# Performance work log

Hardware: AMD Instinct MI355X
Metric: run time of the kernel (lower is better)

## Reference

```python
import jax, jax.numpy as jnp
import numpy as np

B, T, C, H, L = 4, 1024, 1024, 16, 8
Dh = C // H
FF = 4 * C


def _build_mask():
    # init_mask with token_decoder='tokenlearner', prompt=False, block_size=T-1
    block_size = T - 1
    i = np.arange(T)[:, None]
    j = np.arange(T)[None, :]
    tril = j <= i
    # rows i < block_size additionally see cols j of the same 10-unit with j%10 in [0,8]
    unit = 10
    extra = (i < block_size) & (i // unit == j // unit) & (j % unit <= unit - 2)
    return jnp.asarray((tril | extra).astype(np.float32))


def setup_inputs() -> dict:
    key = jax.random.key(0)
    ks = jax.random.split(key, 16)
    s = 0.02
    d = {
        "x": jax.random.normal(ks[0], (B, T, C), jnp.float32),
        "ln1_w": jnp.ones((L, C), jnp.float32),
        "ln1_b": jnp.zeros((L, C), jnp.float32),
        "ln2_w": jnp.ones((L, C), jnp.float32),
        "ln2_b": jnp.zeros((L, C), jnp.float32),
        "wq": s * jax.random.normal(ks[1], (L, C, C), jnp.float32),
        "bq": jnp.zeros((L, C), jnp.float32),
        "wk": s * jax.random.normal(ks[2], (L, C, C), jnp.float32),
        "bk": jnp.zeros((L, C), jnp.float32),
        "wv": s * jax.random.normal(ks[3], (L, C, C), jnp.float32),
        "bv": jnp.zeros((L, C), jnp.float32),
        "wo": s * jax.random.normal(ks[4], (L, C, C), jnp.float32),
        "bo": jnp.zeros((L, C), jnp.float32),
        "w1": s * jax.random.normal(ks[5], (L, C, FF), jnp.float32),
        "b1": jnp.zeros((L, FF), jnp.float32),
        "w2": s * jax.random.normal(ks[6], (L, FF, C), jnp.float32),
        "b2": jnp.zeros((L, C), jnp.float32),
        "mask": _build_mask(),
    }
    return d


def _layer_norm(x, w, b):
    mu = jnp.mean(x, axis=-1, keepdims=True)
    var = jnp.mean(jnp.square(x - mu), axis=-1, keepdims=True)
    return (x - mu) * jax.lax.rsqrt(var + 1e-5) * w + b


def _gpt_stack(x, params, mask):
    neg = jnp.finfo(x.dtype).min
    keep = mask != 0.0  # [T, T]

    def block(xc, p):
        (ln1w, ln1b, ln2w, ln2b, wq, bq, wk, bk, wv, bv,
         wo, bo, w1, b1, w2, b2) = p
        h = _layer_norm(xc, ln1w, ln1b)
        q = (h @ wq + bq).reshape(B, T, H, Dh).transpose(0, 2, 1, 3)
        k = (h @ wk + bk).reshape(B, T, H, Dh).transpose(0, 2, 1, 3)
        v = (h @ wv + bv).reshape(B, T, H, Dh).transpose(0, 2, 1, 3)
        att = jnp.einsum('bhqd,bhkd->bhqk', q, k) * (1.0 / np.sqrt(Dh))
        att = jnp.where(keep[None, None], att, neg)
        att = jax.nn.softmax(att, axis=-1)
        y = jnp.einsum('bhqk,bhkd->bhqd', att, v)
        y = y.transpose(0, 2, 1, 3).reshape(B, T, C)
        xc = xc + y @ wo + bo
        h2 = _layer_norm(xc, ln2w, ln2b)
        m = jax.nn.gelu(h2 @ w1 + b1, approximate=False) @ w2 + b2
        return xc + m

    def step(carry, p):
        return block(carry, p), None

    out, _ = jax.lax.scan(step, x, params)
    return out


def reference(x, ln1_w, ln1_b, ln2_w, ln2_b, wq, bq, wk, bk, wv, bv,
              wo, bo, w1, b1, w2, b2, mask):
    params = (ln1_w, ln1_b, ln2_w, ln2_b, wq, bq, wk, bk, wv, bv,
              wo, bo, w1, b1, w2, b2)
    return _gpt_stack(x, params, mask)
```

## Files before the change

### kernel.cpp

```cpp
#include <hip/hip_runtime.h>

#define TT 1024
#define CC 1024
#define HH 16
#define DHH 64
#define BB 4
#define LL 8
#define FFF 4096
#define MM (BB*TT)

typedef float f32x4 __attribute__((ext_vector_type(4)));
typedef short s16x8 __attribute__((ext_vector_type(8)));
typedef unsigned short u16x8 __attribute__((ext_vector_type(8)));
typedef unsigned short u16x4 __attribute__((ext_vector_type(4)));

__device__ __forceinline__ unsigned short f2bf(float x) {
  unsigned int u = __float_as_uint(x);
  unsigned int r = u + 0x7FFFu + ((u >> 16) & 1u);
  return (unsigned short)(r >> 16);
}
__device__ __forceinline__ float bf2f(unsigned short h) {
  return __uint_as_float(((unsigned int)h) << 16);
}
__device__ __forceinline__ float gelu_f(float x) {
  return 0.5f * x * (1.0f + erff(x * 0.70710678118654752f));
}

struct SplitArgs {
  const float* src[6];
  unsigned short* dh[6];
  unsigned short* dl[6];
};

__global__ __launch_bounds__(256) void splitT_k(SplitArgs a) {
  __shared__ float Ls[64][65];
  int idx = blockIdx.x;
  int r, t;
  if (idx < 1024)      { r = idx >> 8; t = idx & 255; }
  else if (idx < 2048) { r = 4; t = idx - 1024; }
  else                 { r = 5; t = idx - 2048; }
  int K = (r == 5) ? FFF : CC;
  int N = (r == 4) ? FFF : CC;
  int Nt = N >> 6;
  int k0 = (t / Nt) * 64, n0 = (t % Nt) * 64;

  const float* s = a.src[r];
  int tid = threadIdx.x;
  int rrow = tid >> 4, rcol = tid & 15;
#pragma unroll
  for (int i = 0; i < 4; ++i) {
    int rl = rrow + 16 * i;
    float4 v = *(const float4*)(s + (size_t)(k0 + rl) * N + n0 + rcol * 4);
    Ls[rl][rcol * 4 + 0] = v.x; Ls[rl][rcol * 4 + 1] = v.y;
    Ls[rl][rcol * 4 + 2] = v.z; Ls[rl][rcol * 4 + 3] = v.w;
  }
  __syncthreads();

  int nl = tid >> 2, ks = (tid & 3) * 16;
  u16x8 h0, h1, l0, l1;
#pragma unroll
  for (int j = 0; j < 8; ++j) {
    float f = Ls[ks + j][nl];
    h0[j] = f2bf(f); l0[j] = f2bf(f - bf2f(h0[j]));
  }
#pragma unroll
  for (int j = 0; j < 8; ++j) {
    float f = Ls[ks + 8 + j][nl];
    h1[j] = f2bf(f); l1[j] = f2bf(f - bf2f(h1[j]));
  }
  size_t o = (size_t)(n0 + nl) * K + k0 + ks;
  *(u16x8*)(a.dh[r] + o) = h0; *(u16x8*)(a.dh[r] + o + 8) = h1;
  *(u16x8*)(a.dl[r] + o) = l0; *(u16x8*)(a.dl[r] + o + 8) = l1;
}

template <int OUT>
__global__ __launch_bounds__(256) void ln_k(const float* __restrict__ x,
                                            const float* __restrict__ w,
                                            const float* __restrict__ b,
                                            float* __restrict__ of,
                                            unsigned short* __restrict__ oh,
                                            unsigned short* __restrict__ ol) {
  int row = blockIdx.x;
  int tid = threadIdx.x;
  const float* xr = x + (size_t)row * CC;
  float4 v = ((const float4*)xr)[tid];
  float s = v.x + v.y + v.z + v.w;
#pragma unroll
  for (int m = 1; m < 64; m <<= 1) s += __shfl_xor(s, m, 64);
  __shared__ float r1[4];
  __shared__ float r2[4];
  if ((tid & 63) == 0) r1[tid >> 6] = s;
  __syncthreads();
  float mu = (r1[0] + r1[1] + r1[2] + r1[3]) * (1.0f / CC);
  float d0 = v.x - mu, d1 = v.y - mu, d2 = v.z - mu, d3 = v.w - mu;
  float sq = d0 * d0 + d1 * d1 + d2 * d2 + d3 * d3;
#pragma unroll
  for (int m = 1; m < 64; m <<= 1) sq += __shfl_xor(sq, m, 64);
  if ((tid & 63) == 0) r2[tid >> 6] = sq;
  __syncthreads();
  float var = (r2[0] + r2[1] + r2[2] + r2[3]) * (1.0f / CC);
  float rs = rsqrtf(var + 1e-5f);
  float4 wv = ((const float4*)w)[tid];
  float4 bv = ((const float4*)b)[tid];
  float o0 = d0 * rs * wv.x + bv.x;
  float o1 = d1 * rs * wv.y + bv.y;
  float o2 = d2 * rs * wv.z + bv.z;
  float o3 = d3 * rs * wv.w + bv.w;
  if (OUT == 0) {
    float4 ov; ov.x = o0; ov.y = o1; ov.z = o2; ov.w = o3;
    ((float4*)(of + (size_t)row * CC))[tid] = ov;
  } else {
    u16x4 h, lo;
    h[0] = f2bf(o0); lo[0] = f2bf(o0 - bf2f(h[0]));
    h[1] = f2bf(o1); lo[1] = f2bf(o1 - bf2f(h[1]));
    h[2] = f2bf(o2); lo[2] = f2bf(o2 - bf2f(h[2]));
    h[3] = f2bf(o3); lo[3] = f2bf(o3 - bf2f(h[3]));
    *(u16x4*)(oh + (size_t)row * CC + tid * 4) = h;
    *(u16x4*)(ol + (size_t)row * CC + tid * 4) = lo;
  }
}

#define LDA 40

template <int EPI>
__device__ __forceinline__ void sgemm_body(
    const unsigned short* __restrict__ Ah, const unsigned short* __restrict__ Al,
    const unsigned short* __restrict__ Bh, const unsigned short* __restrict__ Bl,
    const float* __restrict__ bias, const float* __restrict__ res,
    float* __restrict__ Cf, unsigned short* __restrict__ Ch,
    unsigned short* __restrict__ Cl,
    int M, int N, int K, int m0, int n0,
    unsigned short* sAh, unsigned short* sAl,
    unsigned short* sBh, unsigned short* sBl) {
  int tid = threadIdx.x;
  int lane = tid & 63;
  int w = tid >> 6;
  int wr = w >> 1, wc = w & 1;
  int l15 = lane & 15, l4 = lane >> 4;

  int sr = tid >> 1, skh = (tid & 1) * 16;
  const unsigned short* ApH = Ah + (size_t)(m0 + sr) * K + skh;
  const unsigned short* ApL = Al + (size_t)(m0 + sr) * K + skh;
  const unsigned short* BpH = Bh + (size_t)(n0 + sr) * K + skh;
  const unsigned short* BpL = Bl + (size_t)(n0 + sr) * K + skh;

  u16x8 rah0 = *(const u16x8*)ApH, rah1 = *(const u16x8*)(ApH + 8);
  u16x8 ral0 = *(const u16x8*)ApL, ral1 = *(const u16x8*)(ApL + 8);
  u16x8 rbh0 = *(const u16x8*)BpH, rbh1 = *(const u16x8*)(BpH + 8);
  u16x8 rbl0 = *(const u16x8*)BpL, rbl1 = *(const u16x8*)(BpL + 8);

  f32x4 acc[4][4];
#pragma unroll
  for (int i = 0; i < 4; ++i)
#pragma unroll
    for (int j = 0; j < 4; ++j) acc[i][j] = {0.f, 0.f, 0.f, 0.f};

  int soff = sr * LDA + skh;
  int nsteps = K >> 5;
  for (int s = 0; s < nsteps; ++s) {
    *(u16x8*)&sAh[soff] = rah0; *(u16x8*)&sAh[soff + 8] = rah1;
    *(u16x8*)&sAl[soff] = ral0; *(u16x8*)&sAl[soff + 8] = ral1;
    *(u16x8*)&sBh[soff] = rbh0; *(u16x8*)&sBh[soff + 8] = rbh1;
    *(u16x8*)&sBl[soff] = rbl0; *(u16x8*)&sBl[soff + 8] = rbl1;
    __syncthreads();

    if (s + 1 < nsteps) {
      int ko = (s + 1) * 32;
      rah0 = *(const u16x8*)(ApH + ko); rah1 = *(const u16x8*)(ApH + ko + 8);
      ral0 = *(const u16x8*)(ApL + ko); ral1 = *(const u16x8*)(ApL + ko + 8);
      rbh0 = *(const u16x8*)(BpH + ko); rbh1 = *(const u16x8*)(BpH + ko + 8);
      rbl0 = *(const u16x8*)(BpL + ko); rbl1 = *(const u16x8*)(BpL + ko + 8);
    }

    s16x8 afh[4], afl[4];
    int ab = (wr * 64 + l15) * LDA + 8 * l4;
#pragma unroll
    for (int mr = 0; mr < 4; ++mr) {
      afh[mr] = *(const s16x8*)&sAh[ab + mr * 16 * LDA];
      afl[mr] = *(const s16x8*)&sAl[ab + mr * 16 * LDA];
    }
    int bb = (wc * 64 + l15) * LDA + 8 * l4;
#pragma unroll
    for (int nr = 0; nr < 4; ++nr) {
      s16x8 bfh = *(const s16x8*)&sBh[bb + nr * 16 * LDA];
      s16x8 bfl = *(const s16x8*)&sBl[bb + nr * 16 * LDA];
#pragma unroll
      for (int mr = 0; mr < 4; ++mr) {
        acc[mr][nr] = __builtin_amdgcn_mfma_f32_16x16x32_bf16(afh[mr], bfh, acc[mr][nr], 0, 0, 0);
        acc[mr][nr] = __builtin_amdgcn_mfma_f32_16x16x32_bf16(afl[mr], bfh, acc[mr][nr], 0, 0, 0);
        acc[mr][nr] = __builtin_amdgcn_mfma_f32_16x16x32_bf16(afh[mr], bfl, acc[mr][nr], 0, 0, 0);
      }
    }
    __syncthreads();
  }

  int row0 = m0 + wr * 64 + l4 * 4;
  int col0 = n0 + wc * 64 + l15;
#pragma unroll
  for (int nr = 0; nr < 4; ++nr) {
    int col = col0 + nr * 16;
    float bv = bias[col];
#pragma unroll
    for (int mr = 0; mr < 4; ++mr) {
#pragma unroll
      for (int r = 0; r < 4; ++r) {
        int row = row0 + mr * 16 + r;
        size_t idx = (size_t)row * N + col;
        float v = acc[mr][nr][r] + bv;
        if (EPI == 0) Cf[idx] = v;
        if (EPI == 1) Cf[idx] = v + res[idx];
        if (EPI == 2) {
          float g = gelu_f(v);
          unsigned short hbits = f2bf(g);
          Ch[idx] = hbits;
          Cl[idx] = f2bf(g - bf2f(hbits));
        }
      }
    }
  }
}

template <int EPI>
__global__ __launch_bounds__(256) void sgemm_k(
    const unsigned short* Ah, const unsigned short* Al,
    const unsigned short* Bh, const unsigned short* Bl,
    const float* bias, const float* res,
    float* Cf, unsigned short* Ch, unsigned short* Cl,
    int M, int N, int K) {
  __shared__ unsigned short sAh[128 * LDA];
  __shared__ unsigned short sAl[128 * LDA];
  __shared__ unsigned short sBh[128 * LDA];
  __shared__ unsigned short sBl[128 * LDA];
  sgemm_body<EPI>(Ah, Al, Bh, Bl, bias, res, Cf, Ch, Cl, M, N, K,
                  blockIdx.y * 128, blockIdx.x * 128, sAh, sAl, sBh, sBl);
}

__global__ __launch_bounds__(256) void sqkv_k(
    const unsigned short* Ah, const unsigned short* Al,
    const unsigned short* wqh, const unsigned short* wql,
    const unsigned short* wkh, const unsigned short* wkl,
    const unsigned short* wvh, const unsigned short* wvl,
    const float* bq, const float* bk, const float* bv,
    float* qo, float* ko, float* vo) {
  __shared__ unsigned short sAh[128 * LDA];
  __shared__ unsigned short sAl[128 * LDA];
  __shared__ unsigned short sBh[128 * LDA];
  __shared__ unsigned short sBl[128 * LDA];
  int which = blockIdx.x >> 3;
  int n0 = (blockIdx.x & 7) * 128;
  const unsigned short* Bh = (which == 0) ? wqh : (which == 1) ? wkh : wvh;
  const unsigned short* Bl = (which == 0) ? wql : (which == 1) ? wkl : wvl;
  const float* bias = (which == 0) ? bq : (which == 1) ? bk : bv;
  float* C = (which == 0) ? qo : (which == 1) ? ko : vo;
  sgemm_body<0>(Ah, Al, Bh, Bl, bias, nullptr, C, nullptr, nullptr,
                MM, CC, CC, blockIdx.y * 128, n0, sAh, sAl, sBh, sBl);
}

#define BK 16
#define LDT 132

template <int EPI>
__device__ __forceinline__ void gemm_body(const float* __restrict__ A,
                                          const float* __restrict__ Bw,
                                          const float* __restrict__ bias,
                                          const float* __restrict__ res,
                                          float* __restrict__ C,
                                          int M, int N, int K,
                                          int m0, int n0,
                                          float (*As)[LDT], float (*Bs)[LDT]) {
  int tid = threadIdx.x;
  int tx = tid & 15, ty = tid >> 4;
  int ar = tid >> 1;
  int aslot = (tid & 1) * 2;
  int brow = tid >> 4;
  int bslot = (tid & 15) * 2;
  const float* Aptr = A + (size_t)(m0 + ar) * K;
  const float* Bptr = Bw + (size_t)brow * N + n0;
  float4 ra0 = ((const float4*)Aptr)[aslot];
  float4 ra1 = ((const float4*)Aptr)[aslot + 1];
  float4 rb0 = ((const float4*)Bptr)[bslot];
  float4 rb1 = ((const float4*)Bptr)[bslot + 1];
  float acc[2][2][4][4] = {};
  for (int k0 = 0; k0 < K; k0 += BK) {
    int ka = aslot * 4;
    As[ka + 0][ar] = ra0.x; As[ka + 1][ar] = ra0.y;
    As[ka + 2][ar] = ra0.z; As[ka + 3][ar] = ra0.w;
    As[ka + 4][ar] = ra1.x; As[ka + 5][ar] = ra1.y;
    As[ka + 6][ar] = ra1.z; As[ka + 7][ar] = ra1.w;
    *(float4*)&Bs[brow][bslot * 4] = rb0;
    *(float4*)&Bs[brow][bslot * 4 + 4] = rb1;
    __syncthreads();
    if (k0 + BK < K) {
      const float* An = Aptr + k0 + BK;
      ra0 = ((const float4*)An)[aslot];
      ra1 = ((const float4*)An)[aslot + 1];
      const float* Bn = Bptr + (size_t)(k0 + BK) * N;
      rb0 = ((const float4*)Bn)[bslot];
      rb1 = ((const float4*)Bn)[bslot + 1];
    }
#pragma unroll
    for (int kk = 0; kk < BK; ++kk) {
      float4 av0 = *(const float4*)&As[kk][ty * 4];
      float4 av1 = *(const float4*)&As[kk][ty * 4 + 64];
      float4 bv0 = *(const float4*)&Bs[kk][tx * 4];
      float4 bv1 = *(const float4*)&Bs[kk][tx * 4 + 64];
      float aa[2][4] = {{av0.x, av0.y, av0.z, av0.w},
                        {av1.x, av1.y, av1.z, av1.w}};
      float bb[2][4] = {{bv0.x, bv0.y, bv0.z, bv0.w},
                        {bv1.x, bv1.y, bv1.z, bv1.w}};
#pragma unroll
      for (int p = 0; p < 2; ++p)
#pragma unroll
        for (int i = 0; i < 4; ++i)
#pragma unroll
          for (int q = 0; q < 2; ++q)
#pragma unroll
            for (int j = 0; j < 4; ++j)
              acc[p][q][i][j] = fmaf(aa[p][i], bb[q][j], acc[p][q][i][j]);
    }
    __syncthreads();
  }
#pragma unroll
  for (int p = 0; p < 2; ++p) {
#pragma unroll
    for (int i = 0; i < 4; ++i) {
      size_t gr = (size_t)(m0 + p * 64 + ty * 4 + i);
      float* Crow = C + gr * N + n0;
#pragma unroll
      for (int q = 0; q < 2; ++q) {
        int c = q * 64 + tx * 4;
        float4 bvv = *(const float4*)&bias[n0 + c];
        float4 o;
        o.x = acc[p][q][i][0] + bvv.x;
        o.y = acc[p][q][i][1] + bvv.y;
        o.z = acc[p][q][i][2] + bvv.z;
        o.w = acc[p][q][i][3] + bvv.w;
        if (EPI == 2) {
          o.x = gelu_f(o.x); o.y = gelu_f(o.y);
          o.z = gelu_f(o.z); o.w = gelu_f(o.w);
        }
        if (EPI == 1) {
          const float* Rrow = res + gr * N + n0;
          float4 rv = *(const float4*)&Rrow[c];
          o.x += rv.x; o.y += rv.y; o.z += rv.z; o.w += rv.w;
        }
        *(float4*)&Crow[c] = o;
      }
    }
  }
}

template <int EPI>
__global__ __launch_bounds__(256) void gemm_k(const float* __restrict__ A,
                                              const float* __restrict__ Bw,
                                              const float* __restrict__ bias,
                                              const float* __restrict__ res,
                                              float* __restrict__ C,
                                              int M, int N, int K) {
  __shared__ float As[BK][LDT];
  __shared__ float Bs[BK][LDT];
  gemm_body<EPI>(A, Bw, bias, res, C, M, N, K,
                 blockIdx.y * 128, blockIdx.x * 128, As, Bs);
}

__global__ __launch_bounds__(256) void qkv_k(const float* __restrict__ A,
                                             const float* __restrict__ wq,
                                             const float* __restrict__ wk,
                                             const float* __restrict__ wv,
                                             const float* __restrict__ bq,
                                             const float* __restrict__ bk,
                                             const float* __restrict__ bv,
                                             float* __restrict__ qo,
                                             float* __restrict__ ko,
                                             float* __restrict__ vo) {
  __shared__ float As[BK][LDT];
  __shared__ float Bs[BK][LDT];
  int which = blockIdx.x >> 3;
  int n0 = (blockIdx.x & 7) * 128;
  const float* Bw = (which == 0) ? wq : (which == 1) ? wk : wv;
  const float* bias = (which == 0) ? bq : (which == 1) ? bk : bv;
  float* C = (which == 0) ? qo : (which == 1) ? ko : vo;
  gemm_body<0>(A, Bw, bias, nullptr, C, MM, CC, CC, blockIdx.y * 128, n0, As, Bs);
}

template <int OUT>
__global__ __launch_bounds__(256) void attn_k(const float* __restrict__ q,
                                              const float* __restrict__ k,
                                              const float* __restrict__ v,
                                              float* __restrict__ yf,
                                              unsigned short* __restrict__ yh,
                                              unsigned short* __restrict__ yl) {
  __shared__ float Qs[64][65];
  __shared__ float KPs[64][65];
  __shared__ float Vs[64][64];

  int tid = threadIdx.x;
  int tx = tid & 15, ty = tid >> 4;
  int qb = blockIdx.x;
  int bh = blockIdx.y;
  int b = bh >> 4;
  int h = bh & 15;
  int q0 = qb * 64;

  const float* qbase = q + (size_t)b * TT * CC + (size_t)h * DHH;
  const float* kbase = k + (size_t)b * TT * CC + (size_t)h * DHH;
  const float* vbase = v + (size_t)b * TT * CC + (size_t)h * DHH;

#pragma unroll
  for (int i = 0; i < 4; ++i) {
    int r = ty + 16 * i;
    float4 t = *(const float4*)(qbase + (size_t)(q0 + r) * CC + tx * 4);
    Qs[r][tx * 4 + 0] = t.x; Qs[r][tx * 4 + 1] = t.y;
    Qs[r][tx * 4 + 2] = t.z; Qs[r][tx * 4 + 3] = t.w;
  }

  float mrun[4], lrun[4], accO[4][4];
#pragma unroll
  for (int i = 0; i < 4; ++i) {
    mrun[i] = -1e30f; lrun[i] = 0.0f;
#pragma unroll
    for (int j = 0; j < 4; ++j) accO[i][j] = 0.0f;
  }

  int kbmax = qb + 1; if (kbmax > (TT / 64 - 1)) kbmax = TT / 64 - 1;
  for (int kb = 0; kb <= kbmax; ++kb) {
    int k0 = kb * 64;
    __syncthreads();
#pragma unroll
    for (int i = 0; i < 4; ++i) {
      int r = ty + 16 * i;
      float4 tk = *(const float4*)(kbase + (size_t)(k0 + r) * CC + tx * 4);
      KPs[r][tx * 4 + 0] = tk.x; KPs[r][tx * 4 + 1] = tk.y;
      KPs[r][tx * 4 + 2] = tk.z; KPs[r][tx * 4 + 3] = tk.w;
      float4 tv = *(const float4*)(vbase + (size_t)(k0 + r) * CC + tx * 4);
      *(float4*)&Vs[r][tx * 4] = tv;
    }
    __syncthreads();

    float s[4][4] = {};
    for (int d = 0; d < 64; ++d) {
      float qv[4], kv[4];
#pragma unroll
      for (int i = 0; i < 4; ++i) qv[i] = Qs[ty * 4 + i][d];
#pragma unroll
      for (int j = 0; j < 4; ++j) kv[j] = KPs[tx * 4 + j][d];
#pragma unroll
      for (int i = 0; i < 4; ++i)
#pragma unroll
        for (int j = 0; j < 4; ++j)
          s[i][j] = fmaf(qv[i], kv[j], s[i][j]);
    }
#pragma unroll
    for (int i = 0; i < 4; ++i) {
      int gi = q0 + ty * 4 + i;
#pragma unroll
      for (int j = 0; j < 4; ++j) {
        int gj = k0 + tx * 4 + j;
        bool keep = (gj <= gi) ||
                    ((gi < TT - 1) && (gi / 10 == gj / 10) && (gj % 10 <= 8));
        s[i][j] = keep ? s[i][j] * 0.125f : -1e30f;
      }
    }
    __syncthreads();

#pragma unroll
    for (int i = 0; i < 4; ++i) {
      float mloc = fmaxf(fmaxf(s[i][0], s[i][1]), fmaxf(s[i][2], s[i][3]));
#pragma unroll
      for (int m = 1; m < 16; m <<= 1) mloc = fmaxf(mloc, __shfl_xor(mloc, m, 64));
      float mnew = fmaxf(mrun[i], mloc);
      float p0 = __expf(s[i][0] - mnew);
      float p1 = __expf(s[i][1] - mnew);
      float p2 = __expf(s[i][2] - mnew);
      float p3 = __expf(s[i][3] - mnew);
      float psum = p0 + p1 + p2 + p3;
#pragma unroll
      for (int m = 1; m < 16; m <<= 1) psum += __shfl_xor(psum, m, 64);
      float alpha = __expf(mrun[i] - mnew);
      lrun[i] = lrun[i] * alpha + psum;
      mrun[i] = mnew;
#pragma unroll
      for (int j = 0; j < 4; ++j) accO[i][j] *= alpha;
      KPs[ty * 4 + i][tx * 4 + 0] = p0;
      KPs[ty * 4 + i][tx * 4 + 1] = p1;
      KPs[ty * 4 + i][tx * 4 + 2] = p2;
      KPs[ty * 4 + i][tx * 4 + 3] = p3;
    }
    __syncthreads();

    for (int c = 0; c < 64; ++c) {
      float pr[4];
#pragma unroll
      for (int i = 0; i < 4; ++i) pr[i] = KPs[ty * 4 + i][c];
      float4 vv = *(const float4*)&Vs[c][tx * 4];
      float vb4[4] = {vv.x, vv.y, vv.z, vv.w};
#pragma unroll
      for (int i = 0; i < 4; ++i)
#pragma unroll
        for (int j = 0; j < 4; ++j)
          accO[i][j] = fmaf(pr[i], vb4[j], accO[i][j]);
    }
  }

#pragma unroll
  for (int i = 0; i < 4; ++i) {
    float inv = 1.0f / lrun[i];
    size_t row = (size_t)(b * TT + q0 + ty * 4 + i);
    int col = h * DHH + tx * 4;
    if (OUT == 0) {
      float4 o;
      o.x = accO[i][0] * inv; o.y = accO[i][1] * inv;
      o.z = accO[i][2] * inv; o.w = accO[i][3] * inv;
      *(float4*)(yf + row * CC + col) = o;
    } else {
      u16x4 hb, lb;
#pragma unroll
      for (int j = 0; j < 4; ++j) {
        float g = accO[i][j] * inv;
        hb[j] = f2bf(g);
        lb[j] = f2bf(g - bf2f(hb[j]));
      }
      *(u16x4*)(yh + row * CC + col) = hb;
      *(u16x4*)(yl + row * CC + col) = lb;
    }
  }
}

extern "C" void kernel_launch(void* const* d_in, const int* in_sizes, int n_in,
                              void* d_out, int out_size, void* d_ws, size_t ws_size,
                              hipStream_t stream) {
  (void)in_sizes; (void)n_in; (void)out_size;
  const float* x    = (const float*)d_in[0];
  const float* ln1w = (const float*)d_in[1];
  const float* ln1b = (const float*)d_in[2];
  const float* ln2w = (const float*)d_in[3];
  const float* ln2b = (const float*)d_in[4];
  const float* wq   = (const float*)d_in[5];
  const float* bq   = (const float*)d_in[6];
  const float* wk   = (const float*)d_in[7];
  const float* bk   = (const float*)d_in[8];
  const float* wv   = (const float*)d_in[9];
  const float* bv   = (const float*)d_in[10];
  const float* wo   = (const float*)d_in[11];
  const float* bo   = (const float*)d_in[12];
  const float* w1   = (const float*)d_in[13];
  const float* b1   = (const float*)d_in[14];
  const float* w2   = (const float*)d_in[15];
  const float* b2   = (const float*)d_in[16];
  float* out = (float*)d_out;

  const size_t SZ = (size_t)MM * CC;
  hipMemcpyAsync(out, x, SZ * sizeof(float), hipMemcpyDeviceToDevice, stream);

  const size_t MB = 1024 * 1024;
  if (ws_size >= 112 * MB) {
    unsigned short* u = (unsigned short*)d_ws;
    const size_t Mu = 1024 * 1024;
    unsigned short* wqh = u;            unsigned short* wql = u + 1 * Mu;
    unsigned short* wkh = u + 2 * Mu;   unsigned short* wkl = u + 3 * Mu;
    unsigned short* wvh = u + 4 * Mu;   unsigned short* wvl = u + 5 * Mu;
    unsigned short* woh = u + 6 * Mu;   unsigned short* wol = u + 7 * Mu;
    unsigned short* w1h = u + 8 * Mu;   unsigned short* w1l = u + 12 * Mu;
    unsigned short* w2h = u + 16 * Mu;  unsigned short* w2l = u + 20 * Mu;
    unsigned short* hh  = u + 24 * Mu;  unsigned short* hl  = u + 28 * Mu;
    float* qf = (float*)(u + 32 * Mu);
    float* kf = qf + 4 * Mu;
    float* vf = kf + 4 * Mu;
    unsigned short* hidh;
    unsigned short* hidl;
    int nch;
    if (ws_size >= 176 * MB) {
      hidh = (unsigned short*)(vf + 4 * Mu);
      hidl = hidh + 16 * Mu;
      nch = 1;
    } else {
      hidh = (unsigned short*)qf;
      hidl = hidh + 8 * Mu;
      nch = 2;
    }
    int mch = MM / nch;

    for (int l = 0; l < LL; ++l) {
      SplitArgs sa;
      sa.src[0] = wq + (size_t)l * CC * CC;  sa.dh[0] = wqh; sa.dl[0] = wql;
      sa.src[1] = wk + (size_t)l * CC * CC;  sa.dh[1] = wkh; sa.dl[1] = wkl;
      sa.src[2] = wv + (size_t)l * CC * CC;  sa.dh[2] = wvh; sa.dl[2] = wvl;
      sa.src[3] = wo + (size_t)l * CC * CC;  sa.dh[3] = woh; sa.dl[3] = wol;
      sa.src[4] = w1 + (size_t)l * CC * FFF; sa.dh[4] = w1h; sa.dl[4] = w1l;
      sa.src[5] = w2 + (size_t)l * FFF * CC; sa.dh[5] = w2h; sa.dl[5] = w2l;
      splitT_k<<<3072, 256, 0, stream>>>(sa);

      ln_k<1><<<MM, 256, 0, stream>>>(out, ln1w + (size_t)l * CC, ln1b + (size_t)l * CC,
                                      nullptr, hh, hl);
      sqkv_k<<<dim3(24, MM / 128), 256, 0, stream>>>(
          hh, hl, wqh, wql, wkh, wkl, wvh, wvl,
          bq + (size_t)l * CC, bk + (size_t)l * CC, bv + (size_t)l * CC,
          qf, kf, vf);
      attn_k<1><<<dim3(TT / 64, BB * HH), 256, 0, stream>>>(qf, kf, vf, nullptr, hh, hl);
      sgemm_k<1><<<dim3(CC / 128, MM / 128), 256, 0, stream>>>(
          hh, hl, woh, wol, bo + (size_t)l * CC, out, out, nullptr, nullptr, MM, CC, CC);
      ln_k<1><<<MM, 256, 0, stream>>>(out, ln2w + (size_t)l * CC, ln2b + (size_t)l * CC,
                                      nullptr, hh, hl);
      for (int c = 0; c < nch; ++c) {
        size_t aoff = (size_t)c * mch * CC;
        sgemm_k<2><<<dim3(FFF / 128, mch / 128), 256, 0, stream>>>(
            hh + aoff, hl + aoff, w1h, w1l, b1 + (size_t)l * FFF, nullptr,
            nullptr, hidh, hidl, mch, FFF, CC);
        sgemm_k<1><<<dim3(CC / 128, mch / 128), 256, 0, stream>>>(
            hidh, hidl, w2h, w2l, b2 + (size_t)l * CC, out + aoff,
            out + aoff, nullptr, nullptr, mch, CC, FFF);
      }
    }
  } else {
    float* hbuf = (float*)d_ws;
    float* qbuf = hbuf + SZ;
    float* kbuf = qbuf + SZ;
    float* vbuf = kbuf + SZ;
    float* hid;
    int nch;
    if (ws_size >= (4 * SZ + (size_t)MM * FFF) * sizeof(float)) {
      hid = vbuf + SZ; nch = 1;
    } else {
      hid = qbuf; nch = 2;
    }
    int mch = MM / nch;
    dim3 gProj(CC / 128, MM / 128);
    for (int l = 0; l < LL; ++l) {
      const float* wq_l = wq + (size_t)l * CC * CC;
      const float* wk_l = wk + (size_t)l * CC * CC;
      const float* wv_l = wv + (size_t)l * CC * CC;
      const float* wo_l = wo + (size_t)l * CC * CC;
      const float* w1_l = w1 + (size_t)l * CC * FFF;
      const float* w2_l = w2 + (size_t)l * FFF * CC;
      ln_k<0><<<MM, 256, 0, stream>>>(out, ln1w + (size_t)l * CC, ln1b + (size_t)l * CC,
                                      hbuf, nullptr, nullptr);
      qkv_k<<<dim3(24, MM / 128), 256, 0, stream>>>(
          hbuf, wq_l, wk_l, wv_l,
          bq + (size_t)l * CC, bk + (size_t)l * CC, bv + (size_t)l * CC,
          qbuf, kbuf, vbuf);
      attn_k<0><<<dim3(TT / 64, BB * HH), 256, 0, stream>>>(qbuf, kbuf, vbuf,
                                                            hbuf, nullptr, nullptr);
      gemm_k<1><<<gProj, 256, 0, stream>>>(hbuf, wo_l, bo + (size_t)l * CC, out, out, MM, CC, CC);
      ln_k<0><<<MM, 256, 0, stream>>>(out, ln2w + (size_t)l * CC, ln2b + (size_t)l * CC,
                                      hbuf, nullptr, nullptr);
      for (int c = 0; c < nch; ++c) {
        const float* aoff = hbuf + (size_t)c * mch * CC;
        float* ooff = out + (size_t)c * mch * CC;
        gemm_k<2><<<dim3(FFF / 128, mch / 128), 256, 0, stream>>>(
            aoff, w1_l, b1 + (size_t)l * FFF, nullptr, hid, mch, FFF, CC);
        gemm_k<1><<<dim3(CC / 128, mch / 128), 256, 0, stream>>>(
            hid, w2_l, b2 + (size_t)l * CC, ooff, ooff, mch, CC, FFF);
      }
    }
  }
}
```

Baseline: 6.004 ms.

## Replace FP32 attention with MFMA split-bf16 flash attention and bf16 QKV outputs

The QKV projection now writes split hi/lo bf16 outputs directly. Q is pre-scaled by 1/sqrt(Dh) and V is stored transposed per head, so a new MFMA-based attention kernel can consume them. The new kernel runs an online-softmax attention per 16-row wave, using three-product split-bf16 MFMAs for both QK^T and PV. It skips key blocks beyond the causal-plus-local mask, which removes the scalar FP32 attention cost and the FP32 QKV round trip. The cost is precision loss from dropping the lo*lo terms, plus uncoalesced transposed-V stores and per-lane global K/V loads with no LDS reuse.

```diff
diff --git a/kernel.cpp b/kernel.cpp
--- a/kernel.cpp
+++ b/kernel.cpp
@@ -196,6 +196,28 @@
 
   int row0 = m0 + wr * 64 + l4 * 4;
   int col0 = n0 + wc * 64 + l15;
+  if (EPI == 5) {
+#pragma unroll
+    for (int nr = 0; nr < 4; ++nr) {
+      int col = col0 + nr * 16;
+      float bv = bias[col];
+#pragma unroll
+      for (int mr = 0; mr < 4; ++mr) {
+        int row = row0 + mr * 16;
+        int t0 = row & (TT - 1);
+        size_t vrow = (size_t)((row >> 10) << 10) + col;
+        u16x4 hb, lb;
+#pragma unroll
+        for (int r = 0; r < 4; ++r) {
+          float v = acc[mr][nr][r] + bv;
+          hb[r] = f2bf(v); lb[r] = f2bf(v - bf2f(hb[r]));
+        }
+        *(u16x4*)(Ch + vrow * TT + t0) = hb;
+        *(u16x4*)(Cl + vrow * TT + t0) = lb;
+      }
+    }
+    return;
+  }
 #pragma unroll
   for (int nr = 0; nr < 4; ++nr) {
     int col = col0 + nr * 16;
@@ -209,8 +231,8 @@
         float v = acc[mr][nr][r] + bv;
         if (EPI == 0) Cf[idx] = v;
         if (EPI == 1) Cf[idx] = v + res[idx];
-        if (EPI == 2) {
-          float g = gelu_f(v);
+        if (EPI == 2 || EPI == 3 || EPI == 4) {
+          float g = (EPI == 2) ? gelu_f(v) : (EPI == 4) ? v * 0.125f : v;
           unsigned short hbits = f2bf(g);
           Ch[idx] = hbits;
           Cl[idx] = f2bf(g - bf2f(hbits));
@@ -241,19 +263,163 @@
     const unsigned short* wkh, const unsigned short* wkl,
     const unsigned short* wvh, const unsigned short* wvl,
     const float* bq, const float* bk, const float* bv,
-    float* qo, float* ko, float* vo) {
+    unsigned short* qhp, unsigned short* qlp,
+    unsigned short* khp, unsigned short* klp,
+    unsigned short* vth, unsigned short* vtl) {
   __shared__ unsigned short sAh[128 * LDA];
   __shared__ unsigned short sAl[128 * LDA];
   __shared__ unsigned short sBh[128 * LDA];
   __shared__ unsigned short sBl[128 * LDA];
   int which = blockIdx.x >> 3;
   int n0 = (blockIdx.x & 7) * 128;
-  const unsigned short* Bh = (which == 0) ? wqh : (which == 1) ? wkh : wvh;
-  const unsigned short* Bl = (which == 0) ? wql : (which == 1) ? wkl : wvl;
-  const float* bias = (which == 0) ? bq : (which == 1) ? bk : bv;
-  float* C = (which == 0) ? qo : (which == 1) ? ko : vo;
-  sgemm_body<0>(Ah, Al, Bh, Bl, bias, nullptr, C, nullptr, nullptr,
-                MM, CC, CC, blockIdx.y * 128, n0, sAh, sAl, sBh, sBl);
+  int m0 = blockIdx.y * 128;
+  if (which == 0) {
+    sgemm_body<4>(Ah, Al, wqh, wql, bq, nullptr, nullptr, qhp, qlp,
+                  MM, CC, CC, m0, n0, sAh, sAl, sBh, sBl);
+  } else if (which == 1) {
+    sgemm_body<3>(Ah, Al, wkh, wkl, bk, nullptr, nullptr, khp, klp,
+                  MM, CC, CC, m0, n0, sAh, sAl, sBh, sBl);
+  } else {
+    sgemm_body<5>(Ah, Al, wvh, wvl, bv, nullptr, nullptr, vth, vtl,
+                  MM, CC, CC, m0, n0, sAh, sAl, sBh, sBl);
+  }
+}
+
+#define LDP 72
+
+__global__ __launch_bounds__(256) void mattn_k(
+    const unsigned short* __restrict__ qh, const unsigned short* __restrict__ ql,
+    const unsigned short* __restrict__ kh, const unsigned short* __restrict__ kl,
+    const unsigned short* __restrict__ vth, const unsigned short* __restrict__ vtl,
+    unsigned short* __restrict__ yh, unsigned short* __restrict__ yl) {
+  __shared__ unsigned short Pbuf[4][2][16 * LDP];
+
+  int tid = threadIdx.x;
+  int lane = tid & 63;
+  int w = tid >> 6;
+  int c = lane & 15, g = lane >> 4;
+  int qb = (int)gridDim.x - 1 - blockIdx.x;
+  int bh = blockIdx.y;
+  int b = bh >> 4, h = bh & 15;
+  int q0w = qb * 64 + w * 16;
+
+  unsigned short* ph = Pbuf[w][0];
+  unsigned short* pl = Pbuf[w][1];
+
+  const size_t qoff = (size_t)(b * TT + q0w + c) * CC + h * DHH + 8 * g;
+  s16x8 qa00 = *(const s16x8*)(qh + qoff);
+  s16x8 qa01 = *(const s16x8*)(ql + qoff);
+  s16x8 qa10 = *(const s16x8*)(qh + qoff + 32);
+  s16x8 qa11 = *(const s16x8*)(ql + qoff + 32);
+
+  int qq[4], qdiv[4];
+#pragma unroll
+  for (int r = 0; r < 4; ++r) { qq[r] = q0w + 4 * g + r; qdiv[r] = qq[r] / 10; }
+
+  float mrun[4], lrun[4];
+  f32x4 accO[4];
+#pragma unroll
+  for (int r = 0; r < 4; ++r) { mrun[r] = -1e30f; lrun[r] = 0.f; }
+#pragma unroll
+  for (int t = 0; t < 4; ++t) accO[t] = {0.f, 0.f, 0.f, 0.f};
+
+  const size_t kbase = (size_t)(b * TT) * CC + h * DHH;
+  const size_t vbase = (size_t)((b * HH + h) * DHH) * TT;
+
+  int kbmax = qb + 1; if (kbmax > TT / 64 - 1) kbmax = TT / 64 - 1;
+  for (int kb = 0; kb <= kbmax; ++kb) {
+    int k0 = kb * 64;
+    if (k0 > q0w + 24) continue;
+
+    f32x4 st[4];
+#pragma unroll
+    for (int nt = 0; nt < 4; ++nt) st[nt] = {0.f, 0.f, 0.f, 0.f};
+#pragma unroll
+    for (int nt = 0; nt < 4; ++nt) {
+      size_t ko = kbase + (size_t)(k0 + nt * 16 + c) * CC + 8 * g;
+      s16x8 kbh0 = *(const s16x8*)(kh + ko);
+      s16x8 kbl0 = *(const s16x8*)(kl + ko);
+      s16x8 kbh1 = *(const s16x8*)(kh + ko + 32);
+      s16x8 kbl1 = *(const s16x8*)(kl + ko + 32);
+      st[nt] = __builtin_amdgcn_mfma_f32_16x16x32_bf16(qa00, kbh0, st[nt], 0, 0, 0);
+      st[nt] = __builtin_amdgcn_mfma_f32_16x16x32_bf16(qa01, kbh0, st[nt], 0, 0, 0);
+      st[nt] = __builtin_amdgcn_mfma_f32_16x16x32_bf16(qa00, kbl0, st[nt], 0, 0, 0);
+      st[nt] = __builtin_amdgcn_mfma_f32_16x16x32_bf16(qa10, kbh1, st[nt], 0, 0, 0);
+      st[nt] = __builtin_amdgcn_mfma_f32_16x16x32_bf16(qa11, kbh1, st[nt], 0, 0, 0);
+      st[nt] = __builtin_amdgcn_mfma_f32_16x16x32_bf16(qa10, kbl1, st[nt], 0, 0, 0);
+    }
+
+    bool full = (k0 + 63 <= q0w);
+    float alpha[4];
+#pragma unroll
+    for (int r = 0; r < 4; ++r) {
+      if (!full) {
+#pragma unroll
+        for (int nt = 0; nt < 4; ++nt) {
+          int kk = k0 + nt * 16 + c;
+          bool keep = (kk <= qq[r]) ||
+                      ((qq[r] < TT - 1) && (qdiv[r] == kk / 10) && (kk % 10 <= 8));
+          if (!keep) st[nt][r] = -1e30f;
+        }
+      }
+      float mm = fmaxf(fmaxf(st[0][r], st[1][r]), fmaxf(st[2][r], st[3][r]));
+      mm = fmaxf(mm, __shfl_xor(mm, 1));
+      mm = fmaxf(mm, __shfl_xor(mm, 2));
+      mm = fmaxf(mm, __shfl_xor(mm, 4));
+      mm = fmaxf(mm, __shfl_xor(mm, 8));
+      float mnew = fmaxf(mrun[r], mm);
+      alpha[r] = __expf(mrun[r] - mnew);
+      mrun[r] = mnew;
+      float ls = 0.f;
+#pragma unroll
+      for (int nt = 0; nt < 4; ++nt) {
+        float p = __expf(st[nt][r] - mnew);
+        ls += p;
+        unsigned short hi = f2bf(p);
+        int po = (4 * g + r) * LDP + nt * 16 + c;
+        ph[po] = hi;
+        pl[po] = f2bf(p - bf2f(hi));
+      }
+      ls += __shfl_xor(ls, 1); ls += __shfl_xor(ls, 2);
+      ls += __shfl_xor(ls, 4); ls += __shfl_xor(ls, 8);
+      lrun[r] = lrun[r] * alpha[r] + ls;
+    }
+#pragma unroll
+    for (int t = 0; t < 4; ++t) {
+      accO[t][0] *= alpha[0]; accO[t][1] *= alpha[1];
+      accO[t][2] *= alpha[2]; accO[t][3] *= alpha[3];
+    }
+
+    asm volatile("s_waitcnt lgkmcnt(0)" ::: "memory");
+
+#pragma unroll
+    for (int ks = 0; ks < 2; ++ks) {
+      s16x8 pah = *(const s16x8*)&ph[c * LDP + 32 * ks + 8 * g];
+      s16x8 pal = *(const s16x8*)&pl[c * LDP + 32 * ks + 8 * g];
+#pragma unroll
+      for (int dvt = 0; dvt < 4; ++dvt) {
+        size_t vo = vbase + (size_t)(dvt * 16 + c) * TT + k0 + 32 * ks + 8 * g;
+        s16x8 vbh = *(const s16x8*)(vth + vo);
+        s16x8 vbl = *(const s16x8*)(vtl + vo);
+        accO[dvt] = __builtin_amdgcn_mfma_f32_16x16x32_bf16(pah, vbh, accO[dvt], 0, 0, 0);
+        accO[dvt] = __builtin_amdgcn_mfma_f32_16x16x32_bf16(pal, vbh, accO[dvt], 0, 0, 0);
+        accO[dvt] = __builtin_amdgcn_mfma_f32_16x16x32_bf16(pah, vbl, accO[dvt], 0, 0, 0);
+      }
+    }
+  }
+
+#pragma unroll
+  for (int r = 0; r < 4; ++r) {
+    float inv = 1.0f / lrun[r];
+    size_t yo = (size_t)(b * TT + qq[r]) * CC + h * DHH;
+#pragma unroll
+    for (int dvt = 0; dvt < 4; ++dvt) {
+      float o = accO[dvt][r] * inv;
+      unsigned short hi = f2bf(o);
+      yh[yo + dvt * 16 + c] = hi;
+      yl[yo + dvt * 16 + c] = f2bf(o - bf2f(hi));
+    }
+  }
 }
 
 #define BK 16
@@ -328,8 +494,8 @@
       float* Crow = C + gr * N + n0;
 #pragma unroll
       for (int q = 0; q < 2; ++q) {
-        int c = q * 64 + tx * 4;
-        float4 bvv = *(const float4*)&bias[n0 + c];
+        int cidx = q * 64 + tx * 4;
+        float4 bvv = *(const float4*)&bias[n0 + cidx];
         float4 o;
         o.x = acc[p][q][i][0] + bvv.x;
         o.y = acc[p][q][i][1] + bvv.y;
@@ -341,10 +507,10 @@
         }
         if (EPI == 1) {
           const float* Rrow = res + gr * N + n0;
-          float4 rv = *(const float4*)&Rrow[c];
+          float4 rv = *(const float4*)&Rrow[cidx];
           o.x += rv.x; o.y += rv.y; o.z += rv.z; o.w += rv.w;
         }
-        *(float4*)&Crow[c] = o;
+        *(float4*)&Crow[cidx] = o;
       }
     }
   }
@@ -383,13 +549,10 @@
   gemm_body<0>(A, Bw, bias, nullptr, C, MM, CC, CC, blockIdx.y * 128, n0, As, Bs);
 }
 
-template <int OUT>
 __global__ __launch_bounds__(256) void attn_k(const float* __restrict__ q,
                                               const float* __restrict__ k,
                                               const float* __restrict__ v,
-                                              float* __restrict__ yf,
-                                              unsigned short* __restrict__ yh,
-                                              unsigned short* __restrict__ yl) {
+                                              float* __restrict__ yf) {
   __shared__ float Qs[64][65];
   __shared__ float KPs[64][65];
   __shared__ float Vs[64][64];
@@ -488,11 +651,11 @@
     }
     __syncthreads();
 
-    for (int c = 0; c < 64; ++c) {
+    for (int cidx = 0; cidx < 64; ++cidx) {
       float pr[4];
 #pragma unroll
-      for (int i = 0; i < 4; ++i) pr[i] = KPs[ty * 4 + i][c];
-      float4 vv = *(const float4*)&Vs[c][tx * 4];
+      for (int i = 0; i < 4; ++i) pr[i] = KPs[ty * 4 + i][cidx];
+      float4 vv = *(const float4*)&Vs[cidx][tx * 4];
       float vb4[4] = {vv.x, vv.y, vv.z, vv.w};
 #pragma unroll
       for (int i = 0; i < 4; ++i)
@@ -505,24 +668,10 @@
 #pragma unroll
   for (int i = 0; i < 4; ++i) {
     float inv = 1.0f / lrun[i];
-    size_t row = (size_t)(b * TT + q0 + ty * 4 + i);
-    int col = h * DHH + tx * 4;
-    if (OUT == 0) {
-      float4 o;
-      o.x = accO[i][0] * inv; o.y = accO[i][1] * inv;
-      o.z = accO[i][2] * inv; o.w = accO[i][3] * inv;
-      *(float4*)(yf + row * CC + col) = o;
-    } else {
-      u16x4 hb, lb;
-#pragma unroll
-      for (int j = 0; j < 4; ++j) {
-        float g = accO[i][j] * inv;
-        hb[j] = f2bf(g);
-        lb[j] = f2bf(g - bf2f(hb[j]));
-      }
-      *(u16x4*)(yh + row * CC + col) = hb;
-      *(u16x4*)(yl + row * CC + col) = lb;
-    }
+    float4 o;
+    o.x = accO[i][0] * inv; o.y = accO[i][1] * inv;
+    o.z = accO[i][2] * inv; o.w = accO[i][3] * inv;
+    *(float4*)(yf + (size_t)(b * TT + q0 + ty * 4 + i) * CC + h * DHH + tx * 4) = o;
   }
 }
 
@@ -563,19 +712,19 @@
     unsigned short* w1h = u + 8 * Mu;   unsigned short* w1l = u + 12 * Mu;
     unsigned short* w2h = u + 16 * Mu;  unsigned short* w2l = u + 20 * Mu;
     unsigned short* hh  = u + 24 * Mu;  unsigned short* hl  = u + 28 * Mu;
-    float* qf = (float*)(u + 32 * Mu);
-    float* kf = qf + 4 * Mu;
-    float* vf = kf + 4 * Mu;
+    unsigned short* qhp = u + 32 * Mu;  unsigned short* qlp = u + 36 * Mu;
+    unsigned short* khp = u + 40 * Mu;  unsigned short* klp = u + 44 * Mu;
+    unsigned short* vth = u + 48 * Mu;  unsigned short* vtl = u + 52 * Mu;
     unsigned short* hidh;
     unsigned short* hidl;
     int nch;
     if (ws_size >= 176 * MB) {
-      hidh = (unsigned short*)(vf + 4 * Mu);
-      hidl = hidh + 16 * Mu;
+      hidh = u + 56 * Mu;
+      hidl = u + 72 * Mu;
       nch = 1;
     } else {
-      hidh = (unsigned short*)qf;
-      hidl = hidh + 8 * Mu;
+      hidh = qhp;
+      hidl = qhp + 8 * Mu;
       nch = 2;
     }
     int mch = MM / nch;
@@ -595,8 +744,9 @@
       sqkv_k<<<dim3(24, MM / 128), 256, 0, stream>>>(
           hh, hl, wqh, wql, wkh, wkl, wvh, wvl,
           bq + (size_t)l * CC, bk + (size_t)l * CC, bv + (size_t)l * CC,
-          qf, kf, vf);
-      attn_k<1><<<dim3(TT / 64, BB * HH), 256, 0, stream>>>(qf, kf, vf, nullptr, hh, hl);
+          qhp, qlp, khp, klp, vth, vtl);
+      mattn_k<<<dim3(TT / 64, BB * HH), 256, 0, stream>>>(
+          qhp, qlp, khp, klp, vth, vtl, hh, hl);
       sgemm_k<1><<<dim3(CC / 128, MM / 128), 256, 0, stream>>>(
           hh, hl, woh, wol, bo + (size_t)l * CC, out, out, nullptr, nullptr, MM, CC, CC);
       ln_k<1><<<MM, 256, 0, stream>>>(out, ln2w + (size_t)l * CC, ln2b + (size_t)l * CC,
@@ -638,8 +788,7 @@
           hbuf, wq_l, wk_l, wv_l,
           bq + (size_t)l * CC, bk + (size_t)l * CC, bv + (size_t)l * CC,
           qbuf, kbuf, vbuf);
-      attn_k<0><<<dim3(TT / 64, BB * HH), 256, 0, stream>>>(qbuf, kbuf, vbuf,
-                                                            hbuf, nullptr, nullptr);
+      attn_k<<<dim3(TT / 64, BB * HH), 256, 0, stream>>>(qbuf, kbuf, vbuf, hbuf);
       gemm_k<1><<<gProj, 256, 0, stream>>>(hbuf, wo_l, bo + (size_t)l * CC, out, out, MM, CC, CC);
       ln_k<0><<<MM, 256, 0, stream>>>(out, ln2w + (size_t)l * CC, ln2b + (size_t)l * CC,
                                       hbuf, nullptr, nullptr);
```

Result: faster. 5.877 ms (-2.1%).
